# Kernel optimization log

Hardware: AMD Instinct MI355X
Metric: run time of the kernel (lower is better)

Reference implementation:

```python
import jax, jax.numpy as jnp
import numpy as np

N, R, A, F, T, O = 50000, 5, 8, 128, 2, 128
RADIUS = 1.0

def _template_vertices():
    # polar grid of template vertices in cartesian coords, shape (R, A, 2)
    radii = (np.arange(1, R + 1) / R) * RADIUS
    angles = np.linspace(0.0, 2.0 * np.pi, A, endpoint=False)
    x = radii[:, None] * np.cos(angles)[None, :]
    y = radii[:, None] * np.sin(angles)[None, :]
    return np.stack([x, y], axis=-1)

def _interp_coeffs():
    # Gaussian interpolation coefficients (concrete define_interpolation_coefficients),
    # shape (R, A, R*A), rows normalized -- constant, non-trainable (built in build()).
    v = _template_vertices().reshape(R * A, 2)
    d2 = ((v[:, None, :] - v[None, :, :]) ** 2).sum(-1)
    sigma = RADIUS / R
    w = np.exp(-d2 / (2.0 * sigma ** 2))
    w = w / w.sum(axis=1, keepdims=True)
    return w.reshape(R, A, R * A).astype(np.float32)

def setup_inputs() -> dict:
    key = jax.random.key(0)
    k1, k2, k3, k4, k5 = jax.random.split(key, 5)
    mesh_signal = jax.random.normal(k1, (N, F), dtype=jnp.float32)
    bary_w = jax.random.uniform(k2, (N, R, A, 3), dtype=jnp.float32)
    bary_w = bary_w / bary_w.sum(axis=-1, keepdims=True)  # barycentric weights sum to 1
    bary_idx = jax.random.randint(k3, (N, R, A, 3), 0, N, dtype=jnp.int32)
    glorot = lambda k, shp: jax.random.uniform(
        k, shp, jnp.float32, -1.0, 1.0) * np.sqrt(6.0 / (shp[-1] + shp[-2]))
    template_weights = glorot(k4, (A, T, O, F))  # (n_angular, templates, out, feat)
    bias = glorot(k5, (T, O))
    return {"mesh_signal": mesh_signal, "bary_w": bary_w,
            "template_weights": template_weights, "bias": bias,
            "interp_coeffs": jnp.asarray(_interp_coeffs()),
            "bary_idx": bary_idx}

def reference(mesh_signal, bary_w, template_weights, bias, interp_coeffs, bary_idx):
    # --- patch operator: barycentric gather + interpolation ---
    gathered = mesh_signal[bary_idx]                       # (N,R,A,3,F) irregular gather
    interp = (bary_w[..., None] * gathered).sum(axis=-2)   # (N,R,A,F)
    # prior: mix all R*A template-vertex signals per output template vertex
    sig = interp.reshape(-1, R * A, F)                     # (N,RA,F)
    interp = jnp.einsum('nkf,rak->nraf', sig, interp_coeffs)  # (N,R,A,F)
    # --- fold: all A rotations (rotation_delta=1), vectorized by rolling weights ---
    rots = jnp.arange(0, A, 1)                             # K = A rotations
    idx = (jnp.arange(A)[None, :] + rots[:, None]) % A     # (K,A): roll(interp,+r) == roll(W,-r)
    W_all = template_weights[idx]                          # (K,A,T,O,F)
    # TF adds bias before summing over (R,A) axes -> bias appears R*A times
    z = jnp.einsum('nraf,katof->nkto', interp, W_all) + (R * A) * bias  # (N,K,T,O)
    out = jax.nn.relu(z).sum(axis=2)                       # sum over templates -> (N,K,O)
    return out
```

## Files before the change

kernel.cpp:

```cpp
#include <hip/hip_runtime.h>
#include <hip/hip_bf16.h>
#include <stdint.h>

#define NN 50000
#define RR 5
#define AA 8
#define FF 128
#define TT 2
#define OO 128
#define KDIM 1024
#define KB 512
#define RA 40

typedef __attribute__((ext_vector_type(8))) short short8;
typedef __attribute__((ext_vector_type(4))) float f32x4;
typedef __attribute__((ext_vector_type(4))) int i32x4;

__device__ inline void gload_lds16(const void* g, void* l) {
  __builtin_amdgcn_global_load_lds(
      (const __attribute__((address_space(1))) unsigned int*)g,
      (__attribute__((address_space(3))) unsigned int*)l, 16, 0, 0);
}

__global__ void prep_kernel(const float* __restrict__ mesh,
                            const float* __restrict__ coeffs,
                            const float* __restrict__ W,
                            const float* __restrict__ bary_w,
                            const int* __restrict__ bary_idx,
                            __hip_bfloat16* __restrict__ meshq,
                            float* __restrict__ G,
                            __hip_bfloat16* __restrict__ Bh,
                            unsigned* __restrict__ packb,
                            int do_pack) {
  int tid = blockIdx.x * blockDim.x + threadIdx.x;
  int stride = gridDim.x * blockDim.x;
  for (int i = tid; i < NN * FF; i += stride) {
    int n = i >> 7, f = i & 127;
    int p = f >> 5, fo = f & 31;
    meshq[((long)p * NN + n) * 32 + fo] = __float2bfloat16(mesh[i]);
  }
  for (int i = tid; i < AA * RA; i += stride) {
    int p = i / RA, k = i % RA;
    int a = p & 3;
    float s1 = 0.f, s2 = 0.f;
    for (int r = 0; r < RR; ++r) {
      s1 += coeffs[(r * AA + a) * RA + k];
      s2 += coeffs[(r * AA + a + 4) * RA + k];
    }
    G[i] = (p < 4) ? (s1 + s2) : (s1 - s2);
  }
  for (int i = tid; i < 2048 * KB; i += stride) {
    int col = i >> 9, k = i & 511;
    int half = col >> 10, c = col & 1023;
    int o = c >> 3, t = (c >> 2) & 1, j = c & 3;
    int a4 = k >> 7, f = k & 127;
    int m = (a4 + j) & 3;
    float w0 = W[((m * TT + t) * OO + o) * FF + f];
    float w4 = W[(((m + 4) * TT + t) * OO + o) * FF + f];
    float v;
    if (half == 0) v = 0.5f * (w0 + w4);
    else {
      v = 0.5f * (w0 - w4);
      if (a4 + j >= 4) v = -v;
    }
    Bh[i] = __float2bfloat16(v);
  }
  if (do_pack) {
    for (int i = tid; i < NN * 120; i += stride) {
      __hip_bfloat16 h = __float2bfloat16(bary_w[i]);
      unsigned wb = *(unsigned short*)&h;
      packb[i] = ((unsigned)bary_idx[i] << 16) | wb;
    }
  }
}

__global__ __launch_bounds__(256) void s_pass_packed(
    const __hip_bfloat16* __restrict__ meshq,
    const unsigned* __restrict__ packb,
    const float* __restrict__ G,
    __hip_bfloat16* __restrict__ Sout,
    int p) {
  __shared__ unsigned pk_s[16 * 120];
  __shared__ float g_s[AA * RA];
  int tid = threadIdx.x;
  long n0 = (long)blockIdx.x * 16;
  const i32x4* psrc = (const i32x4*)(packb + n0 * 120);
  for (int i = tid; i < 480; i += 256) {
    i32x4 v = __builtin_nontemporal_load(psrc + i);
    ((i32x4*)pk_s)[i] = v;
  }
  for (int i = tid; i < AA * RA; i += 256) g_s[i] = G[i];
  __syncthreads();

  int g = tid >> 4;
  int fo = tid & 15;
  long n = n0 + g;
  const unsigned* pg = pk_s + g * 120;
  const char* mbase = (const char*)(meshq + (long)p * NN * 32) + fo * 4;

  float sx_acc[AA], sy_acc[AA];
#pragma unroll
  for (int a = 0; a < AA; ++a) { sx_acc[a] = 0.f; sy_acc[a] = 0.f; }

#pragma unroll 2
  for (int k = 0; k < RA; ++k) {
    float sx = 0.f, sy = 0.f;
#pragma unroll
    for (int j = 0; j < 3; ++j) {
      unsigned v = pg[k * 3 + j];
      unsigned row = v >> 16;
      float w = __uint_as_float(v << 16);
      unsigned u = *(const unsigned*)(mbase + (long)row * 64);
      sx += w * __uint_as_float(u << 16);
      sy += w * __uint_as_float(u & 0xffff0000u);
    }
#pragma unroll
    for (int a = 0; a < AA; ++a) {
      float c = g_s[a * RA + k];
      sx_acc[a] += c * sx;
      sy_acc[a] += c * sy;
    }
  }

  long base = n * KDIM + p * 32 + fo * 2;
#pragma unroll
  for (int a = 0; a < AA; ++a) {
    __hip_bfloat16 hx = __float2bfloat16(sx_acc[a]);
    __hip_bfloat16 hy = __float2bfloat16(sy_acc[a]);
    unsigned u = (unsigned)*(unsigned short*)&hx | ((unsigned)*(unsigned short*)&hy << 16);
    __builtin_nontemporal_store(u, (unsigned*)(Sout + base + a * FF));
  }
}

__global__ __launch_bounds__(256) void s_pass_kernel(
    const __hip_bfloat16* __restrict__ meshq,
    const float* __restrict__ bary_w,
    const int* __restrict__ bary_idx,
    const float* __restrict__ G,
    __hip_bfloat16* __restrict__ Sout,
    int p) {
  __shared__ float w_s[16 * 120];
  __shared__ int i_s[16 * 120];
  __shared__ float g_s[AA * RA];
  int tid = threadIdx.x;
  long n0 = (long)blockIdx.x * 16;
  const f32x4* wsrc = (const f32x4*)(bary_w + n0 * 120);
  const i32x4* isrc = (const i32x4*)(bary_idx + n0 * 120);
  for (int i = tid; i < 480; i += 256) {
    f32x4 wv = __builtin_nontemporal_load(wsrc + i);
    ((f32x4*)w_s)[i] = wv;
    i32x4 iv = __builtin_nontemporal_load(isrc + i);
    ((i32x4*)i_s)[i] = iv;
  }
  for (int i = tid; i < AA * RA; i += 256) g_s[i] = G[i];
  __syncthreads();
  int g = tid >> 4;
  int fo = tid & 15;
  long n = n0 + g;
  const float* wg = w_s + g * 120;
  const int* ig = i_s + g * 120;
  const char* mbase = (const char*)(meshq + (long)p * NN * 32) + fo * 4;
  float sx_acc[AA], sy_acc[AA];
#pragma unroll
  for (int a = 0; a < AA; ++a) { sx_acc[a] = 0.f; sy_acc[a] = 0.f; }
#pragma unroll 2
  for (int k = 0; k < RA; ++k) {
    float sx = 0.f, sy = 0.f;
#pragma unroll
    for (int j = 0; j < 3; ++j) {
      int row = ig[k * 3 + j];
      unsigned u = *(const unsigned*)(mbase + (long)row * 64);
      float w = wg[k * 3 + j];
      sx += w * __uint_as_float(u << 16);
      sy += w * __uint_as_float(u & 0xffff0000u);
    }
#pragma unroll
    for (int a = 0; a < AA; ++a) {
      float c = g_s[a * RA + k];
      sx_acc[a] += c * sx;
      sy_acc[a] += c * sy;
    }
  }
  long base = n * KDIM + p * 32 + fo * 2;
#pragma unroll
  for (int a = 0; a < AA; ++a) {
    __hip_bfloat16 hx = __float2bfloat16(sx_acc[a]);
    __hip_bfloat16 hy = __float2bfloat16(sy_acc[a]);
    unsigned u = (unsigned)*(unsigned short*)&hx | ((unsigned)*(unsigned short*)&hy << 16);
    __builtin_nontemporal_store(u, (unsigned*)(Sout + base + a * FF));
  }
}

__global__ __launch_bounds__(512, 1) void gemm_kernel(
    const __hip_bfloat16* __restrict__ Sh,
    const __hip_bfloat16* __restrict__ Bh,
    const float* __restrict__ bias,
    float* __restrict__ out) {
  int bx = blockIdx.x;
  int by = blockIdx.y;
  int cb = by & 7;
  int mt = ((by >> 3) << 3) + bx;
  if (mt >= 196) return;
  int row0 = mt * 256;
  int cE0 = cb * 128;

  int tid = threadIdx.x;
  int lane = tid & 63;
  int wid = tid >> 6;
  int wave_m = wid >> 2;
  int wave_n = wid & 3;

  __shared__ __align__(16) char lds[147456];

  long srcA[2];
  int dstA[2];
#pragma unroll
  for (int i = 0; i < 2; ++i) {
    int li = i * 512 + tid;
    int r = li >> 2, sp = li & 3;
    int sl = sp ^ ((r >> 1) & 3);
    int rowA = row0 + r;
    if (rowA >= NN) rowA = NN - 1;
    srcA[i] = (long)rowA * KDIM + sl * 8;
    dstA[i] = li * 16;
  }
  long srcB;
  int dstB;
  {
    int r = tid >> 2, sp = tid & 3;
    int sl = sp ^ ((r >> 1) & 3);
    srcB = (long)(cE0 + r) * KB + sl * 8;
    dstB = 32768 + tid * 16;
  }

  int offAE[8], offBE[2];
#pragma unroll
  for (int m = 0; m < 8; ++m) {
    int r = wave_m * 128 + m * 16 + (lane & 15);
    int phys = (lane >> 4) ^ ((r >> 1) & 3);
    offAE[m] = r * 64 + phys * 16;
  }
#pragma unroll
  for (int q = 0; q < 2; ++q) {
    int c = wave_n * 32 + q * 16 + (lane & 15);
    int phys = (lane >> 4) ^ ((c >> 1) & 3);
    offBE[q] = 32768 + c * 64 + phys * 16;
  }

  f32x4 acc[8][4];
#pragma unroll
  for (int m = 0; m < 8; ++m)
#pragma unroll
    for (int q = 0; q < 4; ++q) acc[m][q] = (f32x4){0.f, 0.f, 0.f, 0.f};

#define STAGE(T)                                                              \
  {                                                                           \
    char* base_ = lds + ((T) % 3) * 49152;                                    \
    long k0_ = (long)(T) * 32;                                                \
    _Pragma("unroll") for (int i_ = 0; i_ < 2; ++i_)                          \
        gload_lds16(Sh + srcA[i_] + k0_, base_ + dstA[i_]);                   \
    _Pragma("unroll") for (int i_ = 0; i_ < 2; ++i_)                          \
        gload_lds16(Sh + srcA[i_] + 512 + k0_, base_ + 16384 + dstA[i_]);     \
    gload_lds16(Bh + srcB + k0_, base_ + dstB);                               \
    gload_lds16(Bh + srcB + (long)1024 * KB + k0_, base_ + 8192 + dstB);      \
  }

#define GSTEP(STP, VMSTR, DOSTAGE)                                            \
  {                                                                           \
    const char* cbuf = lds + ((STP) % 3) * 49152;                             \
    asm volatile("s_waitcnt " VMSTR ::: "memory");                            \
    __builtin_amdgcn_sched_barrier(0);                                        \
    __builtin_amdgcn_s_barrier();                                             \
    __builtin_amdgcn_sched_barrier(0);                                        \
    short8 bE[2], bO[2], aE[8], aO[8];                                        \
    _Pragma("unroll") for (int q_ = 0; q_ < 2; ++q_) {                        \
      bE[q_] = *(const short8*)(cbuf + offBE[q_]);                            \
      bO[q_] = *(const short8*)(cbuf + offBE[q_] + 8192);                     \
    }                                                                         \
    _Pragma("unroll") for (int m_ = 0; m_ < 8; ++m_) {                        \
      aE[m_] = *(const short8*)(cbuf + offAE[m_]);                            \
      aO[m_] = *(const short8*)(cbuf + offAE[m_] + 16384);                    \
    }                                                                         \
    if (DOSTAGE) STAGE((STP) + 2)                                             \
    __builtin_amdgcn_s_setprio(1);                                            \
    _Pragma("unroll") for (int m_ = 0; m_ < 8; ++m_) {                        \
      acc[m_][0] = __builtin_amdgcn_mfma_f32_16x16x32_bf16(aE[m_], bE[0],     \
                                                           acc[m_][0], 0, 0, 0); \
      acc[m_][1] = __builtin_amdgcn_mfma_f32_16x16x32_bf16(aE[m_], bE[1],     \
                                                           acc[m_][1], 0, 0, 0); \
      acc[m_][2] = __builtin_amdgcn_mfma_f32_16x16x32_bf16(aO[m_], bO[0],     \
                                                           acc[m_][2], 0, 0, 0); \
      acc[m_][3] = __builtin_amdgcn_mfma_f32_16x16x32_bf16(aO[m_], bO[1],     \
                                                           acc[m_][3], 0, 0, 0); \
    }                                                                         \
    __builtin_amdgcn_s_setprio(0);                                            \
    __builtin_amdgcn_sched_barrier(0);                                        \
  }

  STAGE(0) STAGE(1)
  GSTEP(0, "vmcnt(6)", 1)
  GSTEP(1, "vmcnt(6)", 1)
  GSTEP(2, "vmcnt(6)", 1)
  GSTEP(3, "vmcnt(6)", 1)
  GSTEP(4, "vmcnt(6)", 1)
  GSTEP(5, "vmcnt(6)", 1)
  GSTEP(6, "vmcnt(6)", 1)
  GSTEP(7, "vmcnt(6)", 1)
  GSTEP(8, "vmcnt(6)", 1)
  GSTEP(9, "vmcnt(6)", 1)
  GSTEP(10, "vmcnt(6)", 1)
  GSTEP(11, "vmcnt(6)", 1)
  GSTEP(12, "vmcnt(6)", 1)
  GSTEP(13, "vmcnt(6)", 1)
  GSTEP(14, "vmcnt(6)", 0)
  GSTEP(15, "vmcnt(0)", 0)

  __syncthreads();
  float* lout = (float*)lds;
  int c = lane & 15;
  int t = (c >> 2) & 1;
  int j = c & 3;
  float bq[2];
#pragma unroll
  for (int q = 0; q < 2; ++q) {
    int o = cb * 16 + wave_n * 4 + q * 2 + (c >> 3);
    bq[q] = 40.f * bias[t * OO + o];
  }
#pragma unroll
  for (int m = 0; m < 8; ++m) {
#pragma unroll
    for (int q = 0; q < 2; ++q) {
      int o_l = wave_n * 4 + q * 2 + (c >> 3);
#pragma unroll
      for (int i = 0; i < 4; ++i) {
        float zE = acc[m][q][i];
        float zO = acc[m][q + 2][i];
        float rlo = fmaxf(zE + zO + bq[q], 0.f);
        float rhi = fmaxf(zE - zO + bq[q], 0.f);
        rlo += __shfl_xor(rlo, 4);
        rhi += __shfl_xor(rhi, 4);
        if (!(lane & 4)) {
          int node = wave_m * 128 + m * 16 + (lane >> 4) * 4 + i;
          lout[node * 132 + j * 16 + o_l] = rlo;
          lout[node * 132 + (j + 4) * 16 + o_l] = rhi;
        }
      }
    }
  }
  __syncthreads();

#pragma unroll
  for (int i = 0; i < 16; ++i) {
    int gi = i * 512 + tid;
    int node = gi >> 5;
    int rem = gi & 31;
    int kr = rem >> 2, o4 = rem & 3;
    int grow = row0 + node;
    if (grow < NN) {
      f32x4 v = *(const f32x4*)(lout + node * 132 + kr * 16 + o4 * 4);
      long gaddr = (long)grow * 1024 + kr * 128 + cb * 16 + o4 * 4;
      __builtin_nontemporal_store(v, (f32x4*)(out + gaddr));
    }
  }
}

extern "C" void kernel_launch(void* const* d_in, const int* in_sizes, int n_in,
                              void* d_out, int out_size, void* d_ws, size_t ws_size,
                              hipStream_t stream) {
  const float* mesh   = (const float*)d_in[0];
  const float* bary_w = (const float*)d_in[1];
  const float* W      = (const float*)d_in[2];
  const float* bias   = (const float*)d_in[3];
  const float* coeffs = (const float*)d_in[4];
  const int* bidx     = (const int*)d_in[5];
  float* out = (float*)d_out;
  char* ws = (char*)d_ws;

  __hip_bfloat16* meshq = (__hip_bfloat16*)ws;
  float* G              = (float*)(ws + 12800000);
  __hip_bfloat16* Bh    = (__hip_bfloat16*)(ws + 12801280);
  __hip_bfloat16* Smat  = (__hip_bfloat16*)(ws + 16995584);
  unsigned* packb       = (unsigned*)(ws + 119395584);

  int do_pack = (ws_size >= 143395584UL) ? 1 : 0;

  prep_kernel<<<dim3(2048), dim3(256), 0, stream>>>(mesh, coeffs, W, bary_w, bidx,
                                                    meshq, G, Bh, packb, do_pack);
  if (do_pack) {
    for (int p = 0; p < 4; ++p)
      s_pass_packed<<<dim3(3125), dim3(256), 0, stream>>>(meshq, packb, G, Smat, p);
  } else {
    for (int p = 0; p < 4; ++p)
      s_pass_kernel<<<dim3(3125), dim3(256), 0, stream>>>(meshq, bary_w, bidx, G, Smat, p);
  }
  gemm_kernel<<<dim3(8, 200), dim3(512), 0, stream>>>(Smat, Bh, bias, out);
}
```

Baseline: 430.9 us.

## Fuse four gather passes into one kernel and retile GEMM to 128-row blocks

The four per-slice gather launches are merged into one kernel that loops over the four feature slices, so the packed barycentric data is loaded into LDS once instead of four times. The GEMM moves from 256-thread-pair 256x128 tiles with triple buffering to 256-thread 128x128 tiles with double buffering and two blocks per CU, using full vmcnt(0) waits. The aim is to raise occupancy and cut redundant index loads, at the cost of less prefetch depth per block and a longer-running serial loop per gather thread.

```diff
diff --git a/kernel.cpp b/kernel.cpp
--- a/kernel.cpp
+++ b/kernel.cpp
@@ -74,12 +74,11 @@
   }
 }
 
-__global__ __launch_bounds__(256) void s_pass_packed(
+__global__ __launch_bounds__(256) void s_pass_all(
     const __hip_bfloat16* __restrict__ meshq,
     const unsigned* __restrict__ packb,
     const float* __restrict__ G,
-    __hip_bfloat16* __restrict__ Sout,
-    int p) {
+    __hip_bfloat16* __restrict__ Sout) {
   __shared__ unsigned pk_s[16 * 120];
   __shared__ float g_s[AA * RA];
   int tid = threadIdx.x;
@@ -96,39 +95,39 @@
   int fo = tid & 15;
   long n = n0 + g;
   const unsigned* pg = pk_s + g * 120;
-  const char* mbase = (const char*)(meshq + (long)p * NN * 32) + fo * 4;
-
-  float sx_acc[AA], sy_acc[AA];
-#pragma unroll
-  for (int a = 0; a < AA; ++a) { sx_acc[a] = 0.f; sy_acc[a] = 0.f; }
-
+
+  for (int p = 0; p < 4; ++p) {
+    const char* mbase = (const char*)meshq + (long)p * NN * 64 + fo * 4;
+    float sx_acc[AA], sy_acc[AA];
+#pragma unroll
+    for (int a = 0; a < AA; ++a) { sx_acc[a] = 0.f; sy_acc[a] = 0.f; }
 #pragma unroll 2
-  for (int k = 0; k < RA; ++k) {
-    float sx = 0.f, sy = 0.f;
-#pragma unroll
-    for (int j = 0; j < 3; ++j) {
-      unsigned v = pg[k * 3 + j];
-      unsigned row = v >> 16;
-      float w = __uint_as_float(v << 16);
-      unsigned u = *(const unsigned*)(mbase + (long)row * 64);
-      sx += w * __uint_as_float(u << 16);
-      sy += w * __uint_as_float(u & 0xffff0000u);
-    }
+    for (int k = 0; k < RA; ++k) {
+      float sx = 0.f, sy = 0.f;
+#pragma unroll
+      for (int j = 0; j < 3; ++j) {
+        unsigned v = pg[k * 3 + j];
+        unsigned row = v >> 16;
+        float w = __uint_as_float(v << 16);
+        unsigned u = *(const unsigned*)(mbase + (long)row * 64);
+        sx += w * __uint_as_float(u << 16);
+        sy += w * __uint_as_float(u & 0xffff0000u);
+      }
+#pragma unroll
+      for (int a = 0; a < AA; ++a) {
+        float c = g_s[a * RA + k];
+        sx_acc[a] += c * sx;
+        sy_acc[a] += c * sy;
+      }
+    }
+    long base = n * KDIM + p * 32 + fo * 2;
 #pragma unroll
     for (int a = 0; a < AA; ++a) {
-      float c = g_s[a * RA + k];
-      sx_acc[a] += c * sx;
-      sy_acc[a] += c * sy;
-    }
-  }
-
-  long base = n * KDIM + p * 32 + fo * 2;
-#pragma unroll
-  for (int a = 0; a < AA; ++a) {
-    __hip_bfloat16 hx = __float2bfloat16(sx_acc[a]);
-    __hip_bfloat16 hy = __float2bfloat16(sy_acc[a]);
-    unsigned u = (unsigned)*(unsigned short*)&hx | ((unsigned)*(unsigned short*)&hy << 16);
-    __builtin_nontemporal_store(u, (unsigned*)(Sout + base + a * FF));
+      __hip_bfloat16 hx = __float2bfloat16(sx_acc[a]);
+      __hip_bfloat16 hy = __float2bfloat16(sy_acc[a]);
+      unsigned u = (unsigned)*(unsigned short*)&hx | ((unsigned)*(unsigned short*)&hy << 16);
+      __builtin_nontemporal_store(u, (unsigned*)(Sout + base + a * FF));
+    }
   }
 }
 
@@ -159,7 +158,7 @@
   long n = n0 + g;
   const float* wg = w_s + g * 120;
   const int* ig = i_s + g * 120;
-  const char* mbase = (const char*)(meshq + (long)p * NN * 32) + fo * 4;
+  const char* mbase = (const char*)meshq + (long)p * NN * 64 + fo * 4;
   float sx_acc[AA], sy_acc[AA];
 #pragma unroll
   for (int a = 0; a < AA; ++a) { sx_acc[a] = 0.f; sy_acc[a] = 0.f; }
@@ -191,7 +190,7 @@
   }
 }
 
-__global__ __launch_bounds__(512, 1) void gemm_kernel(
+__global__ __launch_bounds__(256, 2) void gemm_kernel(
     const __hip_bfloat16* __restrict__ Sh,
     const __hip_bfloat16* __restrict__ Bh,
     const float* __restrict__ bias,
@@ -200,149 +199,131 @@
   int by = blockIdx.y;
   int cb = by & 7;
   int mt = ((by >> 3) << 3) + bx;
-  if (mt >= 196) return;
-  int row0 = mt * 256;
+  if (mt >= 391) return;
+  int row0 = mt * 128;
   int cE0 = cb * 128;
 
   int tid = threadIdx.x;
   int lane = tid & 63;
   int wid = tid >> 6;
-  int wave_m = wid >> 2;
-  int wave_n = wid & 3;
-
-  __shared__ __align__(16) char lds[147456];
-
-  long srcA[2];
-  int dstA[2];
+  int wave_m = wid >> 1;
+  int wave_n = wid & 1;
+
+  __shared__ __align__(16) char lds[79872];
+
+  long srcSp[2], srcB[2];
+  int dstA[2], dstBd[2];
 #pragma unroll
   for (int i = 0; i < 2; ++i) {
-    int li = i * 512 + tid;
+    int li = i * 256 + tid;
     int r = li >> 2, sp = li & 3;
     int sl = sp ^ ((r >> 1) & 3);
     int rowA = row0 + r;
     if (rowA >= NN) rowA = NN - 1;
-    srcA[i] = (long)rowA * KDIM + sl * 8;
+    srcSp[i] = (long)rowA * KDIM + sl * 8;
     dstA[i] = li * 16;
-  }
-  long srcB;
-  int dstB;
-  {
-    int r = tid >> 2, sp = tid & 3;
-    int sl = sp ^ ((r >> 1) & 3);
-    srcB = (long)(cE0 + r) * KB + sl * 8;
-    dstB = 32768 + tid * 16;
-  }
-
-  int offAE[8], offBE[2];
-#pragma unroll
-  for (int m = 0; m < 8; ++m) {
-    int r = wave_m * 128 + m * 16 + (lane & 15);
+    srcB[i] = (long)(cE0 + r) * KB + sl * 8;
+    dstBd[i] = 16384 + li * 16;
+  }
+  int offA[4], offB[4];
+#pragma unroll
+  for (int m = 0; m < 4; ++m) {
+    int r = wave_m * 64 + m * 16 + (lane & 15);
     int phys = (lane >> 4) ^ ((r >> 1) & 3);
-    offAE[m] = r * 64 + phys * 16;
-  }
-#pragma unroll
-  for (int q = 0; q < 2; ++q) {
-    int c = wave_n * 32 + q * 16 + (lane & 15);
+    offA[m] = r * 64 + phys * 16;
+  }
+#pragma unroll
+  for (int n = 0; n < 4; ++n) {
+    int c = wave_n * 64 + n * 16 + (lane & 15);
     int phys = (lane >> 4) ^ ((c >> 1) & 3);
-    offBE[q] = 32768 + c * 64 + phys * 16;
-  }
-
-  f32x4 acc[8][4];
-#pragma unroll
-  for (int m = 0; m < 8; ++m)
-#pragma unroll
-    for (int q = 0; q < 4; ++q) acc[m][q] = (f32x4){0.f, 0.f, 0.f, 0.f};
+    offB[n] = 16384 + c * 64 + phys * 16;
+  }
+
+  f32x4 acc[4][8];
+#pragma unroll
+  for (int m = 0; m < 4; ++m)
+#pragma unroll
+    for (int q = 0; q < 8; ++q) acc[m][q] = (f32x4){0.f, 0.f, 0.f, 0.f};
 
 #define STAGE(T)                                                              \
   {                                                                           \
-    char* base_ = lds + ((T) % 3) * 49152;                                    \
+    char* base_ = lds + ((T) & 1) * 32768;                                    \
     long k0_ = (long)(T) * 32;                                                \
     _Pragma("unroll") for (int i_ = 0; i_ < 2; ++i_)                          \
-        gload_lds16(Sh + srcA[i_] + k0_, base_ + dstA[i_]);                   \
+        gload_lds16(Sh + srcSp[i_] + k0_, base_ + dstA[i_]);                  \
     _Pragma("unroll") for (int i_ = 0; i_ < 2; ++i_)                          \
-        gload_lds16(Sh + srcA[i_] + 512 + k0_, base_ + 16384 + dstA[i_]);     \
-    gload_lds16(Bh + srcB + k0_, base_ + dstB);                               \
-    gload_lds16(Bh + srcB + (long)1024 * KB + k0_, base_ + 8192 + dstB);      \
-  }
-
-#define GSTEP(STP, VMSTR, DOSTAGE)                                            \
+        gload_lds16(Sh + srcSp[i_] + 512 + k0_, base_ + 8192 + dstA[i_]);     \
+    _Pragma("unroll") for (int i_ = 0; i_ < 2; ++i_)                          \
+        gload_lds16(Bh + srcB[i_] + k0_, base_ + dstBd[i_]);                  \
+    _Pragma("unroll") for (int i_ = 0; i_ < 2; ++i_)                          \
+        gload_lds16(Bh + srcB[i_] + (long)1024 * KB + k0_,                    \
+                    base_ + 8192 + dstBd[i_]);                                \
+  }
+
+#define GSTEP(STP, DOSTAGE)                                                   \
   {                                                                           \
-    const char* cbuf = lds + ((STP) % 3) * 49152;                             \
-    asm volatile("s_waitcnt " VMSTR ::: "memory");                            \
+    const char* cbuf = lds + ((STP) & 1) * 32768;                             \
+    asm volatile("s_waitcnt vmcnt(0)" ::: "memory");                          \
     __builtin_amdgcn_sched_barrier(0);                                        \
     __builtin_amdgcn_s_barrier();                                             \
     __builtin_amdgcn_sched_barrier(0);                                        \
-    short8 bE[2], bO[2], aE[8], aO[8];                                        \
-    _Pragma("unroll") for (int q_ = 0; q_ < 2; ++q_) {                        \
-      bE[q_] = *(const short8*)(cbuf + offBE[q_]);                            \
-      bO[q_] = *(const short8*)(cbuf + offBE[q_] + 8192);                     \
+    short8 aE[4], aO[4], bE[4], bO[4];                                        \
+    _Pragma("unroll") for (int m_ = 0; m_ < 4; ++m_) {                        \
+      aE[m_] = *(const short8*)(cbuf + offA[m_]);                             \
+      aO[m_] = *(const short8*)(cbuf + offA[m_] + 8192);                      \
     }                                                                         \
-    _Pragma("unroll") for (int m_ = 0; m_ < 8; ++m_) {                        \
-      aE[m_] = *(const short8*)(cbuf + offAE[m_]);                            \
-      aO[m_] = *(const short8*)(cbuf + offAE[m_] + 16384);                    \
+    _Pragma("unroll") for (int n_ = 0; n_ < 4; ++n_) {                        \
+      bE[n_] = *(const short8*)(cbuf + offB[n_]);                             \
+      bO[n_] = *(const short8*)(cbuf + offB[n_] + 8192);                      \
     }                                                                         \
-    if (DOSTAGE) STAGE((STP) + 2)                                             \
+    if (DOSTAGE) STAGE((STP) + 1)                                             \
     __builtin_amdgcn_s_setprio(1);                                            \
-    _Pragma("unroll") for (int m_ = 0; m_ < 8; ++m_) {                        \
-      acc[m_][0] = __builtin_amdgcn_mfma_f32_16x16x32_bf16(aE[m_], bE[0],     \
-                                                           acc[m_][0], 0, 0, 0); \
-      acc[m_][1] = __builtin_amdgcn_mfma_f32_16x16x32_bf16(aE[m_], bE[1],     \
-                                                           acc[m_][1], 0, 0, 0); \
-      acc[m_][2] = __builtin_amdgcn_mfma_f32_16x16x32_bf16(aO[m_], bO[0],     \
-                                                           acc[m_][2], 0, 0, 0); \
-      acc[m_][3] = __builtin_amdgcn_mfma_f32_16x16x32_bf16(aO[m_], bO[1],     \
-                                                           acc[m_][3], 0, 0, 0); \
+    _Pragma("unroll") for (int m_ = 0; m_ < 4; ++m_)                          \
+        _Pragma("unroll") for (int n_ = 0; n_ < 4; ++n_) {                    \
+      acc[m_][n_] = __builtin_amdgcn_mfma_f32_16x16x32_bf16(                  \
+          aE[m_], bE[n_], acc[m_][n_], 0, 0, 0);                              \
+      acc[m_][n_ + 4] = __builtin_amdgcn_mfma_f32_16x16x32_bf16(              \
+          aO[m_], bO[n_], acc[m_][n_ + 4], 0, 0, 0);                          \
     }                                                                         \
     __builtin_amdgcn_s_setprio(0);                                            \
     __builtin_amdgcn_sched_barrier(0);                                        \
   }
 
-  STAGE(0) STAGE(1)
-  GSTEP(0, "vmcnt(6)", 1)
-  GSTEP(1, "vmcnt(6)", 1)
-  GSTEP(2, "vmcnt(6)", 1)
-  GSTEP(3, "vmcnt(6)", 1)
-  GSTEP(4, "vmcnt(6)", 1)
-  GSTEP(5, "vmcnt(6)", 1)
-  GSTEP(6, "vmcnt(6)", 1)
-  GSTEP(7, "vmcnt(6)", 1)
-  GSTEP(8, "vmcnt(6)", 1)
-  GSTEP(9, "vmcnt(6)", 1)
-  GSTEP(10, "vmcnt(6)", 1)
-  GSTEP(11, "vmcnt(6)", 1)
-  GSTEP(12, "vmcnt(6)", 1)
-  GSTEP(13, "vmcnt(6)", 1)
-  GSTEP(14, "vmcnt(6)", 0)
-  GSTEP(15, "vmcnt(0)", 0)
+  STAGE(0)
+  GSTEP(0, 1)  GSTEP(1, 1)  GSTEP(2, 1)  GSTEP(3, 1)
+  GSTEP(4, 1)  GSTEP(5, 1)  GSTEP(6, 1)  GSTEP(7, 1)
+  GSTEP(8, 1)  GSTEP(9, 1)  GSTEP(10, 1) GSTEP(11, 1)
+  GSTEP(12, 1) GSTEP(13, 1) GSTEP(14, 1) GSTEP(15, 0)
 
   __syncthreads();
   float* lout = (float*)lds;
   int c = lane & 15;
   int t = (c >> 2) & 1;
   int j = c & 3;
-  float bq[2];
-#pragma unroll
-  for (int q = 0; q < 2; ++q) {
-    int o = cb * 16 + wave_n * 4 + q * 2 + (c >> 3);
-    bq[q] = 40.f * bias[t * OO + o];
-  }
-#pragma unroll
-  for (int m = 0; m < 8; ++m) {
-#pragma unroll
-    for (int q = 0; q < 2; ++q) {
-      int o_l = wave_n * 4 + q * 2 + (c >> 3);
+  int hi = lane >> 4;
+  float bq[4];
+#pragma unroll
+  for (int n = 0; n < 4; ++n) {
+    int o_l = wave_n * 8 + n * 2 + (c >> 3);
+    bq[n] = 40.f * bias[t * OO + cb * 16 + o_l];
+  }
+#pragma unroll
+  for (int m = 0; m < 4; ++m) {
+#pragma unroll
+    for (int n = 0; n < 4; ++n) {
+      int o_l = wave_n * 8 + n * 2 + (c >> 3);
 #pragma unroll
       for (int i = 0; i < 4; ++i) {
-        float zE = acc[m][q][i];
-        float zO = acc[m][q + 2][i];
-        float rlo = fmaxf(zE + zO + bq[q], 0.f);
-        float rhi = fmaxf(zE - zO + bq[q], 0.f);
+        float zE = acc[m][n][i];
+        float zO = acc[m][n + 4][i];
+        float rlo = fmaxf(zE + zO + bq[n], 0.f);
+        float rhi = fmaxf(zE - zO + bq[n], 0.f);
         rlo += __shfl_xor(rlo, 4);
         rhi += __shfl_xor(rhi, 4);
         if (!(lane & 4)) {
-          int node = wave_m * 128 + m * 16 + (lane >> 4) * 4 + i;
-          lout[node * 132 + j * 16 + o_l] = rlo;
-          lout[node * 132 + (j + 4) * 16 + o_l] = rhi;
+          int node = wave_m * 64 + m * 16 + hi * 4 + i;
+          lout[node * 156 + j * 20 + o_l] = rlo;
+          lout[node * 156 + (j + 4) * 20 + o_l] = rhi;
         }
       }
     }
@@ -350,14 +331,14 @@
   __syncthreads();
 
 #pragma unroll
-  for (int i = 0; i < 16; ++i) {
-    int gi = i * 512 + tid;
+  for (int it = 0; it < 16; ++it) {
+    int gi = it * 256 + tid;
     int node = gi >> 5;
     int rem = gi & 31;
     int kr = rem >> 2, o4 = rem & 3;
     int grow = row0 + node;
     if (grow < NN) {
-      f32x4 v = *(const f32x4*)(lout + node * 132 + kr * 16 + o4 * 4);
+      f32x4 v = *(const f32x4*)(lout + node * 156 + kr * 20 + o4 * 4);
       long gaddr = (long)grow * 1024 + kr * 128 + cb * 16 + o4 * 4;
       __builtin_nontemporal_store(v, (f32x4*)(out + gaddr));
     }
@@ -387,11 +368,10 @@
   prep_kernel<<<dim3(2048), dim3(256), 0, stream>>>(mesh, coeffs, W, bary_w, bidx,
                                                     meshq, G, Bh, packb, do_pack);
   if (do_pack) {
-    for (int p = 0; p < 4; ++p)
-      s_pass_packed<<<dim3(3125), dim3(256), 0, stream>>>(meshq, packb, G, Smat, p);
+    s_pass_all<<<dim3(3125), dim3(256), 0, stream>>>(meshq, packb, G, Smat);
   } else {
     for (int p = 0; p < 4; ++p)
       s_pass_kernel<<<dim3(3125), dim3(256), 0, stream>>>(meshq, bary_w, bidx, G, Smat, p);
   }
-  gemm_kernel<<<dim3(8, 200), dim3(512), 0, stream>>>(Smat, Bh, bias, out);
-}
+  gemm_kernel<<<dim3(8, 392), dim3(256), 0, stream>>>(Smat, Bh, bias, out);
+}
```

New measurement: 455.3 us. +5.7%, slower.
